# Kernel tuning notes

Hardware: AMD Instinct MI355X
Metric: run time of the kernel (lower is better)

Reference implementation:

```python
import jax, jax.numpy as jnp
import numpy as np

NEG_SLOPE = 0.2
EPS = 1e-16


def setup_inputs() -> dict:
    key = jax.random.key(0)
    k1, k2, k3, k4, k5 = jax.random.split(key, 5)
    N, E, F_IN, H, C = 100000, 1600000, 128, 4, 32
    x = jax.random.normal(k1, (N, F_IN), dtype=jnp.float32)
    edge_index = jax.random.randint(k2, (2, E), 0, N, dtype=jnp.int64)
    W = jax.random.normal(k3, (F_IN, H * C), dtype=jnp.float32) * (1.0 / np.sqrt(F_IN))
    att_src = jax.random.normal(k4, (H, C), dtype=jnp.float32) * 0.1
    att_dst = jax.random.normal(k5, (H, C), dtype=jnp.float32) * 0.1
    bias = jnp.zeros((H * C,), dtype=jnp.float32)
    return {"x": x, "edge_index": edge_index, "W": W, "att_src": att_src,
            "att_dst": att_dst, "bias": bias}


def reference(x, edge_index, W, att_src, att_dst, bias):
    N = x.shape[0]
    H, C = att_src.shape
    # PyG GATConv default: add self-loops
    loops = jnp.arange(N, dtype=edge_index.dtype)
    src = jnp.concatenate([edge_index[0], loops])  # [E+N]
    dst = jnp.concatenate([edge_index[1], loops])  # [E+N]

    h = (x @ W).reshape(N, H, C)                  # [N,H,C]
    a_src = jnp.einsum('nhc,hc->nh', h, att_src)  # [N,H]
    a_dst = jnp.einsum('nhc,hc->nh', h, att_dst)  # [N,H]

    e = a_src[src] + a_dst[dst]                   # [E',H]
    e = jax.nn.leaky_relu(e, NEG_SLOPE)

    # segment softmax over destination nodes (numerically stable)
    m = jax.ops.segment_max(e, dst, num_segments=N)      # [N,H]
    p = jnp.exp(e - m[dst])                               # [E',H]
    s = jax.ops.segment_sum(p, dst, num_segments=N)       # [N,H]
    alpha = p / (s[dst] + EPS)                             # [E',H]

    msg = h[src] * alpha[:, :, None]                       # [E',H,C]
    out = jax.ops.segment_sum(msg, dst, num_segments=N)   # [N,H,C]
    return out.reshape(N, H * C) + bias
```

## Files before the change

### kernel.cpp

```cpp
#include <hip/hip_runtime.h>
#include <stdint.h>


#define SLOT 64
#define CNTS 16
#define BCNS 16
#define BCAP 1536
#define MAXB 2048
#define KCH  8192
#define PST  68

typedef __attribute__((ext_vector_type(8))) _Float16 h8;
typedef __attribute__((ext_vector_type(4))) float    f4x;
typedef __attribute__((ext_vector_type(2))) unsigned u32x2;

__device__ __forceinline__ float b2f(unsigned short u) {
    union { unsigned int i; float f; } v; v.i = ((unsigned int)u) << 16; return v.f;
}
__device__ __forceinline__ unsigned short f2b(float f) {
    union { float f; unsigned int i; } v; v.f = f;
    unsigned int i = v.i;
    unsigned int r = (i + 0x7FFFu + ((i >> 16) & 1u)) >> 16;
    return (unsigned short)r;
}
__device__ __forceinline__ unsigned short f2h(float f) {
    union { _Float16 h; unsigned short u; } v; v.h = (_Float16)f; return v.u;
}
__device__ __forceinline__ float h2f(unsigned short u) {
    union { _Float16 h; unsigned short u; } v; v.u = u; return (float)v.h;
}

__device__ __forceinline__ int edge_at(const int* idx32, const long long* idx64,
                                       int is64, long long pos) {
    return is64 ? (int)idx64[pos] : idx32[pos];
}

__global__ void k_prep(const void* __restrict__ Wv, const void* __restrict__ asv,
                       const void* __restrict__ adv, const void* __restrict__ bv,
                       const int* __restrict__ eidx, const unsigned int* __restrict__ xw,
                       int* __restrict__ flags,
                       _Float16* __restrict__ Wth, _Float16* __restrict__ Wtl,
                       float* __restrict__ attf , float* __restrict__ biasf ,
                       int* __restrict__ bcnt, int nbcnt ) {
    __shared__ int nz, bf;
    int tid = threadIdx.x;
    if (tid == 0) { nz = 0; bf = 0; }
    __syncthreads();
    int hits = 0;
    for (int i = tid; i < 4096; i += 256) {
        unsigned int e = (xw[i] >> 7) & 0xFFu;
        if (e >= 0x60u && e < 0xA0u) ++hits;
    }
    atomicAdd(&bf, hits);
    if (blockIdx.x == 0) {
        int bad = 0;
        for (int i = tid; i < 1024; i += 256)
            if (eidx[2 * i + 1] != 0) bad = 1;
        if (bad) atomicOr(&nz, 1);
    }
    __syncthreads();
    int isbf = (bf > 3072) ? 1 : 0;
    if (blockIdx.x == 0 && tid == 0) {
        flags[0] = (nz == 0) ? 1 : 0;
        flags[1] = isbf;
    }
    for (int i = blockIdx.x * 256 + tid; i < nbcnt; i += gridDim.x * 256)
        bcnt[i] = 0;
    int gtid = blockIdx.x * 256 + tid;
    for (int i = gtid; i < 16384; i += gridDim.x * 256) {
        int col = i >> 7, k = i & 127;
        float w = isbf ? b2f(((const unsigned short*)Wv)[k * 128 + col])
                       : ((const float*)Wv)[k * 128 + col];
        unsigned short hi = f2h(w);
        unsigned short lo = f2h(w - h2f(hi));
        ((unsigned short*)Wth)[i] = hi;
        ((unsigned short*)Wtl)[i] = lo;
    }
    if (blockIdx.x == 0) {
        for (int i = tid; i < 128; i += 256) {
            attf[i]       = isbf ? b2f(((const unsigned short*)asv)[i]) : ((const float*)asv)[i];
            attf[128 + i] = isbf ? b2f(((const unsigned short*)adv)[i]) : ((const float*)adv)[i];
            biasf[i]      = isbf ? b2f(((const unsigned short*)bv)[i]) : ((const float*)bv)[i];
        }
    }
}

__global__ __launch_bounds__(256) void k_gemm_scatter(
    const void* __restrict__ xv,
    const _Float16* __restrict__ Wth, const _Float16* __restrict__ Wtl,
    const float* __restrict__ attf, const int* __restrict__ flags,
    unsigned short* __restrict__ hbf, float* __restrict__ asf,
    float* __restrict__ adf, int N,
    const int* __restrict__ idx32, const long long* __restrict__ idx64,
    int* __restrict__ bcnt, unsigned* __restrict__ bdat,
    int* __restrict__ cnt, int* __restrict__ esrc,
    int E, int Gg, int SB) {
    __shared__ unsigned short xsh[64 * 128];
    __shared__ unsigned short xsl[64 * 128];
    int tid = threadIdx.x;
    int bid = blockIdx.x;

    if (bid < SB) {
        int is64 = flags[0];
        int NBK = (N + 63) >> 6;
        long long e0 = (long long)bid * KCH;
        long long e1 = e0 + KCH; if (e1 > E) e1 = E;
        if (e0 >= E) return;

        if (NBK <= MAXB) {
            int wid = tid >> 6;
            int* h0 = (int*)xsh; int* h1 = h0 + MAXB;
            int* h2 = (int*)xsl; int* h3 = h2 + MAXB;
            int* hw = (wid == 0) ? h0 : (wid == 1) ? h1 : (wid == 2) ? h2 : h3;
            for (int i = tid; i < NBK; i += 256) { h0[i] = 0; h1[i] = 0; h2[i] = 0; h3[i] = 0; }
            __syncthreads();
            for (long long e = e0 + tid; e < e1; e += 256) {
                int d = is64 ? (int)idx64[(long long)E + e] : idx32[E + e];
                atomicAdd(&hw[d >> 6], 1);
            }
            __syncthreads();
            for (int b = tid; b < NBK; b += 256) {
                int c0 = h0[b], c1 = h1[b], c2 = h2[b], c3 = h3[b];
                int t = c0 + c1 + c2 + c3;
                int base = (t > 0) ? atomicAdd(&bcnt[(size_t)b * BCNS], t) : 0;
                h0[b] = base;
                h1[b] = base + c0;
                h2[b] = base + c0 + c1;
                h3[b] = base + c0 + c1 + c2;
            }
            __syncthreads();
            for (long long e = e0 + tid; e < e1; e += 256) {
                int d, s;
                if (is64) {
                    d = (int)idx64[(long long)E + e]; s = (int)idx64[e];
                } else {
                    d = idx32[E + e]; s = idx32[e];
                }
                int b = d >> 6;
                int p = atomicAdd(&hw[b], 1);
                if (p < BCAP)
                    bdat[(size_t)b * BCAP + p] = (unsigned)s | ((unsigned)(d & 63) << 26);
            }
        } else {
            for (long long e = e0 + tid; e < e1; e += 256) {
                int d = edge_at(idx32, idx64, is64, (long long)E + e);
                int s = edge_at(idx32, idx64, is64, e);
                int p = atomicAdd(&cnt[(size_t)d * CNTS], 1);
                if (p < SLOT) esrc[(size_t)d * SLOT + p] = s;
            }
        }
        return;
    }

    int rb = bid - SB;
    if (rb >= Gg) return;
    int r0 = rb * 64;
    int isbf = flags[1];
    int w = tid >> 6;
    int lane = tid & 63;
    int li = lane & 15;
    int g  = lane >> 4;
    int c0 = w * 32;

    h8 Bh[2][4], Bl[2][4];
#pragma unroll
    for (int t = 0; t < 2; ++t)
#pragma unroll
        for (int s = 0; s < 4; ++s) {
            size_t o = (size_t)(c0 + 16 * t + li) * 128 + 32 * s + 8 * g;
            Bh[t][s] = *(const h8*)(Wth + o);
            Bl[t][s] = *(const h8*)(Wtl + o);
        }

#pragma unroll
    for (int it = 0; it < 4; ++it) {
        int idx = it * 2048 + tid * 8;
        int r = idx >> 7, k = idx & 127;
        int gr = r0 + r; if (gr >= N) gr = N - 1;
        float v[8];
        if (isbf) {
            uint4 raw = *(const uint4*)((const unsigned short*)xv + (size_t)gr * 128 + k);
            v[0] = b2f((unsigned short)(raw.x & 0xFFFFu)); v[1] = b2f((unsigned short)(raw.x >> 16));
            v[2] = b2f((unsigned short)(raw.y & 0xFFFFu)); v[3] = b2f((unsigned short)(raw.y >> 16));
            v[4] = b2f((unsigned short)(raw.z & 0xFFFFu)); v[5] = b2f((unsigned short)(raw.z >> 16));
            v[6] = b2f((unsigned short)(raw.w & 0xFFFFu)); v[7] = b2f((unsigned short)(raw.w >> 16));
        } else {
            const float* xf = (const float*)xv;
            float4 a = *(const float4*)(xf + (size_t)gr * 128 + k);
            float4 b = *(const float4*)(xf + (size_t)gr * 128 + k + 4);
            v[0] = a.x; v[1] = a.y; v[2] = a.z; v[3] = a.w;
            v[4] = b.x; v[5] = b.y; v[6] = b.z; v[7] = b.w;
        }
        uint4 PH, PL;
        unsigned int ph[4], pl[4];
#pragma unroll
        for (int jj = 0; jj < 4; ++jj) {
            unsigned short h0 = f2h(v[2 * jj]), h1 = f2h(v[2 * jj + 1]);
            unsigned short l0 = f2h(v[2 * jj] - h2f(h0));
            unsigned short l1 = f2h(v[2 * jj + 1] - h2f(h1));
            ph[jj] = (unsigned int)h0 | ((unsigned int)h1 << 16);
            pl[jj] = (unsigned int)l0 | ((unsigned int)l1 << 16);
        }
        PH.x = ph[0]; PH.y = ph[1]; PH.z = ph[2]; PH.w = ph[3];
        PL.x = pl[0]; PL.y = pl[1]; PL.z = pl[2]; PL.w = pl[3];
        int off = r * 256 + ((2 * k) ^ ((r & 7) << 4));
        *(uint4*)((char*)xsh + off) = PH;
        *(uint4*)((char*)xsl + off) = PL;
    }
    __syncthreads();

    f4x acc[4][2];
#pragma unroll
    for (int m = 0; m < 4; ++m)
#pragma unroll
        for (int t = 0; t < 2; ++t) acc[m][t] = (f4x){0.f, 0.f, 0.f, 0.f};

#pragma unroll
    for (int s = 0; s < 4; ++s) {
#pragma unroll
        for (int m = 0; m < 4; ++m) {
            int row = 16 * m + li;
            int kb = (32 * s + 8 * g) * 2;
            int off = row * 256 + (kb ^ ((row & 7) << 4));
            h8 ah = *(const h8*)((const char*)xsh + off);
            h8 al = *(const h8*)((const char*)xsl + off);
#pragma unroll
            for (int t = 0; t < 2; ++t) {
                acc[m][t] = __builtin_amdgcn_mfma_f32_16x16x32_f16(ah, Bh[t][s], acc[m][t], 0, 0, 0);
                acc[m][t] = __builtin_amdgcn_mfma_f32_16x16x32_f16(al, Bh[t][s], acc[m][t], 0, 0, 0);
                acc[m][t] = __builtin_amdgcn_mfma_f32_16x16x32_f16(ah, Bl[t][s], acc[m][t], 0, 0, 0);
            }
        }
    }

    float at_s0 = attf[c0 + li],       at_s1 = attf[c0 + 16 + li];
    float at_d0 = attf[128 + c0 + li], at_d1 = attf[128 + c0 + 16 + li];
#pragma unroll
    for (int m = 0; m < 4; ++m) {
        float s1v[4], s2v[4];
#pragma unroll
        for (int j = 0; j < 4; ++j) {
            s1v[j] = acc[m][0][j] * at_s0 + acc[m][1][j] * at_s1;
            s2v[j] = acc[m][0][j] * at_d0 + acc[m][1][j] * at_d1;
        }
#pragma unroll
        for (int j = 0; j < 4; ++j) {
#pragma unroll
            for (int msk = 1; msk < 16; msk <<= 1) {
                s1v[j] += __shfl_xor(s1v[j], msk);
                s2v[j] += __shfl_xor(s2v[j], msk);
            }
        }
        if (li == 0) {
#pragma unroll
            for (int j = 0; j < 4; ++j) {
                int gr = r0 + 16 * m + 4 * g + j;
                if (gr < N) {
                    asf[(size_t)gr * 4 + w] = s1v[j];
                    adf[(size_t)gr * 4 + w] = s2v[j];
                }
            }
        }
    }

    __syncthreads();
#pragma unroll
    for (int m = 0; m < 4; ++m)
#pragma unroll
        for (int t = 0; t < 2; ++t)
#pragma unroll
            for (int j = 0; j < 4; ++j)
                xsh[(16 * m + 4 * g + j) * 128 + c0 + 16 * t + li] = f2b(acc[m][t][j]);
    __syncthreads();
#pragma unroll
    for (int it = 0; it < 4; ++it) {
        int u = it * 2048 + tid * 8;
        int r = u >> 7, k = u & 127;
        int gr = r0 + r;
        if (gr < N)
            *(uint4*)(hbf + (size_t)gr * 128 + k) = *(const uint4*)(xsh + u);
    }
}

template <int NB>
__device__ __forceinline__ void agg_node2(
    int n, int dl, int deg, int lane,
    const int lslot[64][SLOT], float* psh,
    const unsigned short* __restrict__ hbf,
    const float* __restrict__ asf, const float* __restrict__ adf,
    float a[4], float& invho) {
    int half = lane >> 5;
    int cl = lane & 31;
    int hd = cl >> 3;
    int sl = (lane == 0) ? n : ((lane <= deg) ? lslot[dl][lane - 1] : n);
    float4 av, adv;
    asm volatile("global_load_dwordx4 %0, %1, off"
                 : "=v"(av) : "v"((const void*)(asf + (size_t)sl * 4)));
    asm volatile("global_load_dwordx4 %0, %1, off"
                 : "=v"(adv) : "v"((const void*)(adf + (size_t)n * 4)));
    u32x2 vv[NB * 8];
#pragma unroll
    for (int k = 0; k < NB * 8; ++k) {
        int it = 2 * k + half;
        int s = (it == 0) ? n : ((it <= deg) ? lslot[dl][it - 1] : n);
        asm volatile("global_load_dwordx2 %0, %1, off"
                     : "=v"(vv[k]) : "v"((const void*)(hbf + (size_t)s * 128 + 4 * cl)));
    }
    asm volatile("s_waitcnt vmcnt(%0)" :: "n"(NB * 8));
    __builtin_amdgcn_sched_barrier(0);

    float p0 = 0.f, p1 = 0.f, p2 = 0.f, p3 = 0.f;
    if (lane <= deg) {
        float e0 = av.x + adv.x; e0 = fmaxf(e0, 0.2f * e0); p0 = __expf(e0);
        float e1 = av.y + adv.y; e1 = fmaxf(e1, 0.2f * e1); p1 = __expf(e1);
        float e2 = av.z + adv.z; e2 = fmaxf(e2, 0.2f * e2); p2 = __expf(e2);
        float e3 = av.w + adv.w; e3 = fmaxf(e3, 0.2f * e3); p3 = __expf(e3);
    }
    psh[0 * PST + lane] = p0; psh[1 * PST + lane] = p1;
    psh[2 * PST + lane] = p2; psh[3 * PST + lane] = p3;
    __builtin_amdgcn_wave_barrier();
    asm volatile("s_waitcnt lgkmcnt(0)" ::: "memory");
    __builtin_amdgcn_wave_barrier();

    float ps0 = p0, ps1 = p1, ps2 = p2, ps3 = p3;
#pragma unroll
    for (int m = 1; m < 64; m <<= 1) {
        ps0 += __shfl_xor(ps0, m);
        ps1 += __shfl_xor(ps1, m);
        ps2 += __shfl_xor(ps2, m);
        ps3 += __shfl_xor(ps3, m);
    }
    float den = hd == 0 ? ps0 : hd == 1 ? ps1 : hd == 2 ? ps2 : ps3;
    invho = 1.0f / (den + 1e-16f);

#pragma unroll
    for (int bi = 0; bi < NB; ++bi) {
        asm volatile("s_waitcnt vmcnt(%0)" :: "n"(8 * (NB - 1 - bi)));
        __builtin_amdgcn_sched_barrier(0);
#pragma unroll
        for (int k2 = 0; k2 < 8; ++k2) {
            int it = 2 * (bi * 8 + k2) + half;
            float q = psh[hd * PST + it];
            u32x2 v = vv[bi * 8 + k2];
            a[0] += q * b2f((unsigned short)v[0]);
            a[1] += q * b2f((unsigned short)(v[0] >> 16));
            a[2] += q * b2f((unsigned short)v[1]);
            a[3] += q * b2f((unsigned short)(v[1] >> 16));
        }
    }
}

__global__ __launch_bounds__(256) void k_bagg(
    const unsigned* __restrict__ bdat, const int* __restrict__ bcnt,
    const unsigned short* __restrict__ hbf,
    const float* __restrict__ asf, const float* __restrict__ adf,
    const int* __restrict__ idx32, const long long* __restrict__ idx64,
    const float* __restrict__ biasf, const int* __restrict__ flags,
    void* __restrict__ outv, int N, int E) {
    __shared__ int   lcnt[64];
    __shared__ int   lslot[64][SLOT];
    __shared__ float p_all[4][4 * PST];
    int b = blockIdx.x >> 1;
    int bh = blockIdx.x & 1;
    int tid = threadIdx.x;
    int wid = tid >> 6, lane = tid & 63, head = lane >> 4;

    if (tid < 64) lcnt[tid] = 0;
    __syncthreads();
    int mm = bcnt[(size_t)b * BCNS];
    int ovf = (mm > BCAP);
    if (mm > BCAP) mm = BCAP;
    for (int i = tid; i < mm; i += 256) {
        unsigned e = bdat[(size_t)b * BCAP + i];
        int dl = (int)(e >> 26);
        int p = atomicAdd(&lcnt[dl], 1);
        if (p < SLOT) lslot[dl][p] = (int)(e & 0x03FFFFFFu);
    }
    __syncthreads();

    int cl = lane & 31;
    float b0 = biasf[2 * lane], b1 = biasf[2 * lane + 1];
    float4 bq4 = *(const float4*)(biasf + 4 * cl);
    float* psh = p_all[wid];
    int isbf = flags[1];
    int is64 = flags[0];

    for (int u = 0; u < 8; ++u) {
        int dl = bh * 32 + wid * 8 + u;
        int n = (b << 6) + dl;
        if (n >= N) break;
        int deg = lcnt[dl];
        bool fb = ovf || (deg > SLOT - 1);

        if (!fb && deg <= 31) {
            float a4[4] = {0.f, 0.f, 0.f, 0.f};
            float invh = 0.f;
            int nb = (deg + 16) >> 4;
            if (nb == 1) agg_node2<1>(n, dl, deg, lane, lslot, psh, hbf, asf, adf, a4, invh);
            else         agg_node2<2>(n, dl, deg, lane, lslot, psh, hbf, asf, adf, a4, invh);
#pragma unroll
            for (int c = 0; c < 4; ++c) a4[c] += __shfl_xor(a4[c], 32);
            float o0 = a4[0] * invh + bq4.x, o1 = a4[1] * invh + bq4.y;
            float o2 = a4[2] * invh + bq4.z, o3 = a4[3] * invh + bq4.w;
            if (lane < 32) {
                if (isbf) {
                    u32x2 pk;
                    pk[0] = (unsigned)f2b(o0) | ((unsigned)f2b(o1) << 16);
                    pk[1] = (unsigned)f2b(o2) | ((unsigned)f2b(o3) << 16);
                    *(u32x2*)((unsigned*)outv + (size_t)n * 64 + cl * 2) = pk;
                } else {
                    float4 f4v; f4v.x = o0; f4v.y = o1; f4v.z = o2; f4v.w = o3;
                    *(float4*)((float*)outv + (size_t)n * 128 + cl * 4) = f4v;
                }
            }
        } else if (!fb) {
            float a0 = 0.f, a1 = 0.f;
            float4 adv = *(const float4*)(adf + (size_t)n * 4);
            int sl = (lane == 0) ? n : ((lane <= deg) ? lslot[dl][lane - 1] : n);
            float4 av = *(const float4*)(asf + (size_t)sl * 4);
            float p0 = 0.f, p1 = 0.f, p2 = 0.f, p3 = 0.f;
            if (lane <= deg) {
                float e0 = av.x + adv.x; e0 = fmaxf(e0, 0.2f * e0); p0 = __expf(e0);
                float e1 = av.y + adv.y; e1 = fmaxf(e1, 0.2f * e1); p1 = __expf(e1);
                float e2 = av.z + adv.z; e2 = fmaxf(e2, 0.2f * e2); p2 = __expf(e2);
                float e3 = av.w + adv.w; e3 = fmaxf(e3, 0.2f * e3); p3 = __expf(e3);
            }
            psh[0 * PST + lane] = p0; psh[1 * PST + lane] = p1;
            psh[2 * PST + lane] = p2; psh[3 * PST + lane] = p3;
            __builtin_amdgcn_wave_barrier();
            asm volatile("s_waitcnt lgkmcnt(0)" ::: "memory");
            __builtin_amdgcn_wave_barrier();
            float ps0 = p0, ps1 = p1, ps2 = p2, ps3 = p3;
#pragma unroll
            for (int m = 1; m < 64; m <<= 1) {
                ps0 += __shfl_xor(ps0, m);
                ps1 += __shfl_xor(ps1, m);
                ps2 += __shfl_xor(ps2, m);
                ps3 += __shfl_xor(ps3, m);
            }
            float den = head == 0 ? ps0 : head == 1 ? ps1 : head == 2 ? ps2 : ps3;
            float invh = 1.0f / (den + 1e-16f);
            int nb = (deg + 8) >> 3;
            for (int bi = 0; bi < nb; ++bi) {
                unsigned vt[8];
#pragma unroll
                for (int k2 = 0; k2 < 8; ++k2) {
                    int it = bi * 8 + k2;
                    int s = (it == 0) ? n : ((it <= deg) ? lslot[dl][it - 1] : n);
                    vt[k2] = *(const unsigned int*)(hbf + (size_t)s * 128 + 2 * lane);
                }
#pragma unroll
                for (int k2 = 0; k2 < 8; ++k2) {
                    float q = psh[head * PST + bi * 8 + k2];
                    a0 += q * b2f((unsigned short)vt[k2]);
                    a1 += q * b2f((unsigned short)(vt[k2] >> 16));
                }
            }
            a0 = a0 * invh + b0;
            a1 = a1 * invh + b1;
            if (isbf) {
                unsigned int pk = (unsigned int)f2b(a0) | ((unsigned int)f2b(a1) << 16);
                ((unsigned int*)outv)[(size_t)n * 64 + lane] = pk;
            } else {
                float2 f2; f2.x = a0; f2.y = a1;
                *(float2*)((float*)outv + (size_t)n * 128 + 2 * lane) = f2;
            }
        } else {
            float a0 = 0.f, a1 = 0.f;
            float4 adv = *(const float4*)(adf + (size_t)n * 4);
            float adh = head == 0 ? adv.x : head == 1 ? adv.y : head == 2 ? adv.z : adv.w;
            float den = 0.f;
            {
                float ev = asf[(size_t)n * 4 + head] + adh; ev = fmaxf(ev, 0.2f * ev);
                float p = __expf(ev);
                unsigned int v = *(const unsigned int*)(hbf + (size_t)n * 128 + 2 * lane);
                den += p;
                a0 += p * b2f((unsigned short)v);
                a1 += p * b2f((unsigned short)(v >> 16));
            }
            for (int e = 0; e < E; ++e) {
                int d = edge_at(idx32, idx64, is64, (long long)E + e);
                if (d == n) {
                    int s = edge_at(idx32, idx64, is64, e);
                    float ev = asf[(size_t)s * 4 + head] + adh; ev = fmaxf(ev, 0.2f * ev);
                    float p = __expf(ev);
                    unsigned int v = *(const unsigned int*)(hbf + (size_t)s * 128 + 2 * lane);
                    den += p;
                    a0 += p * b2f((unsigned short)v);
                    a1 += p * b2f((unsigned short)(v >> 16));
                }
            }
            float invh = 1.0f / (den + 1e-16f);
            a0 = a0 * invh + b0;
            a1 = a1 * invh + b1;
            if (isbf) {
                unsigned int pk = (unsigned int)f2b(a0) | ((unsigned int)f2b(a1) << 16);
                ((unsigned int*)outv)[(size_t)n * 64 + lane] = pk;
            } else {
                float2 f2; f2.x = a0; f2.y = a1;
                *(float2*)((float*)outv + (size_t)n * 128 + 2 * lane) = f2;
            }
        }
        __builtin_amdgcn_wave_barrier();
    }
}

__global__ __launch_bounds__(256) void k_aggregate(
    const unsigned short* __restrict__ hbf,
    const float* __restrict__ asf, const float* __restrict__ adf,
    const int* __restrict__ cnt, const int* __restrict__ esrc,
    const int* __restrict__ idx32, const long long* __restrict__ idx64,
    const float* __restrict__ biasf, const int* __restrict__ flags,
    void* __restrict__ outv, int N, int E) {
    __shared__ float p_sh_all[4][SLOT * 4];
    __shared__ int   s_sh_all[4][SLOT];
    int wid = threadIdx.x >> 6;
    int lane = threadIdx.x & 63;
    int n = blockIdx.x * 4 + wid;
    if (n >= N) n = N - 1;
    float* p_sh = p_sh_all[wid];
    int*   s_sh = s_sh_all[wid];
    int head = lane >> 4;

    int deg = cnt[(size_t)n * CNTS];
    float4 adv = *(const float4*)(adf + (size_t)n * 4);
    bool fb = (deg > SLOT - 1);

    float p0 = 0.f, p1 = 0.f, p2 = 0.f, p3 = 0.f;
    if (!fb && lane <= deg) {
        int s = (lane == 0) ? n : esrc[(size_t)n * SLOT + lane - 1];
        float4 av = *(const float4*)(asf + (size_t)s * 4);
        float e0 = av.x + adv.x; e0 = fmaxf(e0, 0.2f * e0); p0 = __expf(e0);
        float e1 = av.y + adv.y; e1 = fmaxf(e1, 0.2f * e1); p1 = __expf(e1);
        float e2 = av.z + adv.z; e2 = fmaxf(e2, 0.2f * e2); p2 = __expf(e2);
        float e3 = av.w + adv.w; e3 = fmaxf(e3, 0.2f * e3); p3 = __expf(e3);
        s_sh[lane] = s;
        p_sh[lane * 4 + 0] = p0; p_sh[lane * 4 + 1] = p1;
        p_sh[lane * 4 + 2] = p2; p_sh[lane * 4 + 3] = p3;
    }
    __syncthreads();

    float b0 = biasf[2 * lane], b1 = biasf[2 * lane + 1];
    float a0 = 0.f, a1 = 0.f, invh;

    if (!fb) {
        float ps0 = p0, ps1 = p1, ps2 = p2, ps3 = p3;
#pragma unroll
        for (int m = 1; m < 64; m <<= 1) {
            ps0 += __shfl_xor(ps0, m);
            ps1 += __shfl_xor(ps1, m);
            ps2 += __shfl_xor(ps2, m);
            ps3 += __shfl_xor(ps3, m);
        }
        float den = head == 0 ? ps0 : head == 1 ? ps1 : head == 2 ? ps2 : ps3;
        invh = 1.0f / (den + 1e-16f);

        int tot = deg + 1;
        int i = 0;
        for (; i + 3 < tot; i += 4) {
            int s0 = s_sh[i], s1 = s_sh[i + 1], s2 = s_sh[i + 2], s3 = s_sh[i + 3];
            float q0 = p_sh[i * 4 + head],       q1 = p_sh[(i + 1) * 4 + head];
            float q2 = p_sh[(i + 2) * 4 + head], q3 = p_sh[(i + 3) * 4 + head];
            unsigned int v0 = *(const unsigned int*)(hbf + (size_t)s0 * 128 + 2 * lane);
            unsigned int v1 = *(const unsigned int*)(hbf + (size_t)s1 * 128 + 2 * lane);
            unsigned int v2 = *(const unsigned int*)(hbf + (size_t)s2 * 128 + 2 * lane);
            unsigned int v3 = *(const unsigned int*)(hbf + (size_t)s3 * 128 + 2 * lane);
            a0 += q0 * b2f((unsigned short)v0) + q1 * b2f((unsigned short)v1)
                + q2 * b2f((unsigned short)v2) + q3 * b2f((unsigned short)v3);
            a1 += q0 * b2f((unsigned short)(v0 >> 16)) + q1 * b2f((unsigned short)(v1 >> 16))
                + q2 * b2f((unsigned short)(v2 >> 16)) + q3 * b2f((unsigned short)(v3 >> 16));
        }
        for (; i < tot; ++i) {
            int s0 = s_sh[i];
            float q0 = p_sh[i * 4 + head];
            unsigned int v0 = *(const unsigned int*)(hbf + (size_t)s0 * 128 + 2 * lane);
            a0 += q0 * b2f((unsigned short)v0);
            a1 += q0 * b2f((unsigned short)(v0 >> 16));
        }
    } else {
        int is64 = flags[0];
        float adh = head == 0 ? adv.x : head == 1 ? adv.y : head == 2 ? adv.z : adv.w;
        float den = 0.f;
        {
            float ev = asf[(size_t)n * 4 + head] + adh; ev = fmaxf(ev, 0.2f * ev);
            float p = __expf(ev);
            unsigned int v = *(const unsigned int*)(hbf + (size_t)n * 128 + 2 * lane);
            den += p;
            a0 += p * b2f((unsigned short)v);
            a1 += p * b2f((unsigned short)(v >> 16));
        }
        for (int e = 0; e < E; ++e) {
            int d = edge_at(idx32, idx64, is64, (long long)E + e);
            if (d == n) {
                int s = edge_at(idx32, idx64, is64, e);
                float ev = asf[(size_t)s * 4 + head] + adh; ev = fmaxf(ev, 0.2f * ev);
                float p = __expf(ev);
                unsigned int v = *(const unsigned int*)(hbf + (size_t)s * 128 + 2 * lane);
                den += p;
                a0 += p * b2f((unsigned short)v);
                a1 += p * b2f((unsigned short)(v >> 16));
            }
        }
        invh = 1.0f / (den + 1e-16f);
    }

    a0 = a0 * invh + b0;
    a1 = a1 * invh + b1;
    if (flags[1]) {
        unsigned int pk = (unsigned int)f2b(a0) | ((unsigned int)f2b(a1) << 16);
        ((unsigned int*)outv)[(size_t)n * 64 + lane] = pk;
    } else {
        float2 f2; f2.x = a0; f2.y = a1;
        *(float2*)((float*)outv + (size_t)n * 128 + 2 * lane) = f2;
    }
}

extern "C" void kernel_launch(void* const* d_in, const int* in_sizes, int n_in,
                              void* d_out, int out_size, void* d_ws, size_t ws_size,
                              hipStream_t stream) {
    const void*      xv    = d_in[0];
    const int*       idx32 = (const int*)d_in[1];
    const long long* idx64 = (const long long*)d_in[1];

    int N = in_sizes[0] / 128;
    int E = in_sizes[1] / 2;

    char* ws = (char*)d_ws;
    size_t o = 0;
    auto alloc = [&](size_t bytes) {
        size_t r = o; o += (bytes + 255) & ~(size_t)255; return r;
    };
    unsigned short* hbf = (unsigned short*)(ws + alloc((size_t)N * 128 * 2));
    _Float16* Wth = (_Float16*)(ws + alloc(16384 * 2));
    _Float16* Wtl = (_Float16*)(ws + alloc(16384 * 2));
    float* attf  = (float*)(ws + alloc(256 * 4));
    float* biasf = (float*)(ws + alloc(128 * 4));
    float* asf   = (float*)(ws + alloc((size_t)N * 4 * 4));
    float* adf   = (float*)(ws + alloc((size_t)N * 4 * 4));
    int* cnt     = (int*)(ws + alloc((size_t)N * CNTS * 4));
    int* flags   = (int*)(ws + alloc(256));
    int* esrc    = (int*)(ws + alloc((size_t)N * SLOT * 4));
    int NBK = (N + 63) >> 6;
    int* bcnt      = (int*)(ws + alloc((size_t)NBK * BCNS * 4));
    unsigned* bdat = (unsigned*)(ws + alloc((size_t)NBK * BCAP * 4));

    int Gg = (N + 63) / 64;
    int SB = (E + KCH - 1) / KCH;
    int NB = SB + Gg;

    k_prep<<<16, 256, 0, stream>>>(d_in[2], d_in[3], d_in[4], d_in[5],
                                   idx32, (const unsigned int*)xv, flags,
                                   Wth, Wtl, attf, biasf,
                                   bcnt, (NBK <= MAXB) ? NBK * BCNS : 0);
    if (NBK <= MAXB) {
        k_gemm_scatter<<<NB, 256, 0, stream>>>(xv, Wth, Wtl, attf, flags, hbf, asf, adf, N,
                                               idx32, idx64, bcnt, bdat, cnt, esrc, E, Gg, SB);
        k_bagg<<<NBK * 2, 256, 0, stream>>>(bdat, bcnt, hbf, asf, adf, idx32, idx64,
                                            biasf, flags, d_out, N, E);
    } else {
        hipMemsetAsync(cnt, 0, (size_t)N * CNTS * 4, stream);
        k_gemm_scatter<<<NB, 256, 0, stream>>>(xv, Wth, Wtl, attf, flags, hbf, asf, adf, N,
                                               idx32, idx64, bcnt, bdat, cnt, esrc, E, Gg, SB);
        k_aggregate<<<(N + 3) / 4, 256, 0, stream>>>(hbf, asf, adf, cnt, esrc, idx32, idx64,
                                                     biasf, flags, d_out, N, E);
    }
}
```

Baseline: 253.3 us.

## Process two destination nodes per wave with interleaved gather loads

```diff
diff --git a/kernel.cpp b/kernel.cpp
--- a/kernel.cpp
+++ b/kernel.cpp
@@ -350,7 +350,244 @@
     }
 }
 
-__global__ __launch_bounds__(256) void k_bagg(
+template <int NBA, int NBB>
+__device__ __forceinline__ void agg_node2_dual(
+    int nA, int dlA, int degA, int nB, int dlB, int degB, int lane,
+    const int lslot[64][SLOT], float* pshA, float* pshB,
+    const unsigned short* __restrict__ hbf,
+    const float* __restrict__ asf, const float* __restrict__ adf,
+    float aA[4], float aB[4], float& invhA, float& invhB) {
+    int half = lane >> 5;
+    int cl = lane & 31;
+    int hd = cl >> 3;
+    int slA = (lane == 0) ? nA : ((lane <= degA) ? lslot[dlA][lane - 1] : nA);
+    float4 avA, adA;
+    asm volatile("global_load_dwordx4 %0, %1, off"
+                 : "=v"(avA) : "v"((const void*)(asf + (size_t)slA * 4)));
+    asm volatile("global_load_dwordx4 %0, %1, off"
+                 : "=v"(adA) : "v"((const void*)(adf + (size_t)nA * 4)));
+    u32x2 vvA[NBA * 8];
+#pragma unroll
+    for (int k = 0; k < NBA * 8; ++k) {
+        int it = 2 * k + half;
+        int s = (it == 0) ? nA : ((it <= degA) ? lslot[dlA][it - 1] : nA);
+        asm volatile("global_load_dwordx2 %0, %1, off"
+                     : "=v"(vvA[k]) : "v"((const void*)(hbf + (size_t)s * 128 + 4 * cl)));
+    }
+    int slB = (lane == 0) ? nB : ((lane <= degB) ? lslot[dlB][lane - 1] : nB);
+    float4 avB, adB;
+    asm volatile("global_load_dwordx4 %0, %1, off"
+                 : "=v"(avB) : "v"((const void*)(asf + (size_t)slB * 4)));
+    asm volatile("global_load_dwordx4 %0, %1, off"
+                 : "=v"(adB) : "v"((const void*)(adf + (size_t)nB * 4)));
+    u32x2 vvB[NBB * 8];
+#pragma unroll
+    for (int k = 0; k < NBB * 8; ++k) {
+        int it = 2 * k + half;
+        int s = (it == 0) ? nB : ((it <= degB) ? lslot[dlB][it - 1] : nB);
+        asm volatile("global_load_dwordx2 %0, %1, off"
+                     : "=v"(vvB[k]) : "v"((const void*)(hbf + (size_t)s * 128 + 4 * cl)));
+    }
+    asm volatile("s_waitcnt vmcnt(%0)" :: "n"(NBA * 8 + NBB * 8 + 2));
+    __builtin_amdgcn_sched_barrier(0);
+    float pA0 = 0.f, pA1 = 0.f, pA2 = 0.f, pA3 = 0.f;
+    if (lane <= degA) {
+        float e0 = avA.x + adA.x; e0 = fmaxf(e0, 0.2f * e0); pA0 = __expf(e0);
+        float e1 = avA.y + adA.y; e1 = fmaxf(e1, 0.2f * e1); pA1 = __expf(e1);
+        float e2 = avA.z + adA.z; e2 = fmaxf(e2, 0.2f * e2); pA2 = __expf(e2);
+        float e3 = avA.w + adA.w; e3 = fmaxf(e3, 0.2f * e3); pA3 = __expf(e3);
+    }
+    pshA[0 * PST + lane] = pA0; pshA[1 * PST + lane] = pA1;
+    pshA[2 * PST + lane] = pA2; pshA[3 * PST + lane] = pA3;
+    asm volatile("s_waitcnt vmcnt(%0)" :: "n"(NBB * 8));
+    __builtin_amdgcn_sched_barrier(0);
+    float pB0 = 0.f, pB1 = 0.f, pB2 = 0.f, pB3 = 0.f;
+    if (lane <= degB) {
+        float e0 = avB.x + adB.x; e0 = fmaxf(e0, 0.2f * e0); pB0 = __expf(e0);
+        float e1 = avB.y + adB.y; e1 = fmaxf(e1, 0.2f * e1); pB1 = __expf(e1);
+        float e2 = avB.z + adB.z; e2 = fmaxf(e2, 0.2f * e2); pB2 = __expf(e2);
+        float e3 = avB.w + adB.w; e3 = fmaxf(e3, 0.2f * e3); pB3 = __expf(e3);
+    }
+    pshB[0 * PST + lane] = pB0; pshB[1 * PST + lane] = pB1;
+    pshB[2 * PST + lane] = pB2; pshB[3 * PST + lane] = pB3;
+    __builtin_amdgcn_wave_barrier();
+    asm volatile("s_waitcnt lgkmcnt(0)" ::: "memory");
+    __builtin_amdgcn_wave_barrier();
+
+    float sA0 = pA0, sA1 = pA1, sA2 = pA2, sA3 = pA3;
+    float sB0 = pB0, sB1 = pB1, sB2 = pB2, sB3 = pB3;
+#pragma unroll
+    for (int m = 1; m < 64; m <<= 1) {
+        sA0 += __shfl_xor(sA0, m); sB0 += __shfl_xor(sB0, m);
+        sA1 += __shfl_xor(sA1, m); sB1 += __shfl_xor(sB1, m);
+        sA2 += __shfl_xor(sA2, m); sB2 += __shfl_xor(sB2, m);
+        sA3 += __shfl_xor(sA3, m); sB3 += __shfl_xor(sB3, m);
+    }
+    float denA = hd == 0 ? sA0 : hd == 1 ? sA1 : hd == 2 ? sA2 : sA3;
+    float denB = hd == 0 ? sB0 : hd == 1 ? sB1 : hd == 2 ? sB2 : sB3;
+    invhA = 1.0f / (denA + 1e-16f);
+    invhB = 1.0f / (denB + 1e-16f);
+
+#pragma unroll
+    for (int bi = 0; bi < NBA; ++bi) {
+        asm volatile("s_waitcnt vmcnt(%0)" :: "n"(8 * (NBA - 1 - bi) + NBB * 8 + 2));
+        __builtin_amdgcn_sched_barrier(0);
+#pragma unroll
+        for (int k2 = 0; k2 < 8; ++k2) {
+            int it = 2 * (bi * 8 + k2) + half;
+            float q = pshA[hd * PST + it];
+            u32x2 v = vvA[bi * 8 + k2];
+            aA[0] += q * b2f((unsigned short)v[0]);
+            aA[1] += q * b2f((unsigned short)(v[0] >> 16));
+            aA[2] += q * b2f((unsigned short)v[1]);
+            aA[3] += q * b2f((unsigned short)(v[1] >> 16));
+        }
+    }
+#pragma unroll
+    for (int bi = 0; bi < NBB; ++bi) {
+        asm volatile("s_waitcnt vmcnt(%0)" :: "n"(8 * (NBB - 1 - bi)));
+        __builtin_amdgcn_sched_barrier(0);
+#pragma unroll
+        for (int k2 = 0; k2 < 8; ++k2) {
+            int it = 2 * (bi * 8 + k2) + half;
+            float q = pshB[hd * PST + it];
+            u32x2 v = vvB[bi * 8 + k2];
+            aB[0] += q * b2f((unsigned short)v[0]);
+            aB[1] += q * b2f((unsigned short)(v[0] >> 16));
+            aB[2] += q * b2f((unsigned short)v[1]);
+            aB[3] += q * b2f((unsigned short)(v[1] >> 16));
+        }
+    }
+}
+
+__device__ __forceinline__ void bagg_store_fast(
+    void* outv, int n, int lane, int cl, int isbf,
+    const float a4in[4], float invh, float4 bq4) {
+    float a0 = a4in[0], a1 = a4in[1], a2 = a4in[2], a3 = a4in[3];
+    a0 += __shfl_xor(a0, 32); a1 += __shfl_xor(a1, 32);
+    a2 += __shfl_xor(a2, 32); a3 += __shfl_xor(a3, 32);
+    float o0 = a0 * invh + bq4.x, o1 = a1 * invh + bq4.y;
+    float o2 = a2 * invh + bq4.z, o3 = a3 * invh + bq4.w;
+    if (lane < 32) {
+        if (isbf) {
+            u32x2 pk;
+            pk[0] = (unsigned)f2b(o0) | ((unsigned)f2b(o1) << 16);
+            pk[1] = (unsigned)f2b(o2) | ((unsigned)f2b(o3) << 16);
+            *(u32x2*)((unsigned*)outv + (size_t)n * 64 + cl * 2) = pk;
+        } else {
+            float4 f4v; f4v.x = o0; f4v.y = o1; f4v.z = o2; f4v.w = o3;
+            *(float4*)((float*)outv + (size_t)n * 128 + cl * 4) = f4v;
+        }
+    }
+}
+
+__device__ void bagg_one(
+    int n, int dl, int deg, bool fb,
+    int lane, int head, int cl,
+    const int lslot[64][SLOT], float* psh,
+    const unsigned short* __restrict__ hbf,
+    const float* __restrict__ asf, const float* __restrict__ adf,
+    const int* __restrict__ idx32, const long long* __restrict__ idx64,
+    float b0, float b1, float4 bq4, int isbf, int is64,
+    void* __restrict__ outv, int N, int E) {
+    if (!fb && deg <= 31) {
+        float a4[4] = {0.f, 0.f, 0.f, 0.f};
+        float invh = 0.f;
+        int nb = (deg + 16) >> 4;
+        if (nb == 1) agg_node2<1>(n, dl, deg, lane, lslot, psh, hbf, asf, adf, a4, invh);
+        else         agg_node2<2>(n, dl, deg, lane, lslot, psh, hbf, asf, adf, a4, invh);
+        bagg_store_fast(outv, n, lane, cl, isbf, a4, invh, bq4);
+    } else if (!fb) {
+        float a0 = 0.f, a1 = 0.f;
+        float4 adv = *(const float4*)(adf + (size_t)n * 4);
+        int sl = (lane == 0) ? n : ((lane <= deg) ? lslot[dl][lane - 1] : n);
+        float4 av = *(const float4*)(asf + (size_t)sl * 4);
+        float p0 = 0.f, p1 = 0.f, p2 = 0.f, p3 = 0.f;
+        if (lane <= deg) {
+            float e0 = av.x + adv.x; e0 = fmaxf(e0, 0.2f * e0); p0 = __expf(e0);
+            float e1 = av.y + adv.y; e1 = fmaxf(e1, 0.2f * e1); p1 = __expf(e1);
+            float e2 = av.z + adv.z; e2 = fmaxf(e2, 0.2f * e2); p2 = __expf(e2);
+            float e3 = av.w + adv.w; e3 = fmaxf(e3, 0.2f * e3); p3 = __expf(e3);
+        }
+        psh[0 * PST + lane] = p0; psh[1 * PST + lane] = p1;
+        psh[2 * PST + lane] = p2; psh[3 * PST + lane] = p3;
+        __builtin_amdgcn_wave_barrier();
+        asm volatile("s_waitcnt lgkmcnt(0)" ::: "memory");
+        __builtin_amdgcn_wave_barrier();
+        float ps0 = p0, ps1 = p1, ps2 = p2, ps3 = p3;
+#pragma unroll
+        for (int m = 1; m < 64; m <<= 1) {
+            ps0 += __shfl_xor(ps0, m);
+            ps1 += __shfl_xor(ps1, m);
+            ps2 += __shfl_xor(ps2, m);
+            ps3 += __shfl_xor(ps3, m);
+        }
+        float den = head == 0 ? ps0 : head == 1 ? ps1 : head == 2 ? ps2 : ps3;
+        float invh = 1.0f / (den + 1e-16f);
+        int nb = (deg + 8) >> 3;
+        for (int bi = 0; bi < nb; ++bi) {
+            unsigned vt[8];
+#pragma unroll
+            for (int k2 = 0; k2 < 8; ++k2) {
+                int it = bi * 8 + k2;
+                int s = (it == 0) ? n : ((it <= deg) ? lslot[dl][it - 1] : n);
+                vt[k2] = *(const unsigned int*)(hbf + (size_t)s * 128 + 2 * lane);
+            }
+#pragma unroll
+            for (int k2 = 0; k2 < 8; ++k2) {
+                float q = psh[head * PST + bi * 8 + k2];
+                a0 += q * b2f((unsigned short)vt[k2]);
+                a1 += q * b2f((unsigned short)(vt[k2] >> 16));
+            }
+        }
+        a0 = a0 * invh + b0;
+        a1 = a1 * invh + b1;
+        if (isbf) {
+            unsigned int pk = (unsigned int)f2b(a0) | ((unsigned int)f2b(a1) << 16);
+            ((unsigned int*)outv)[(size_t)n * 64 + lane] = pk;
+        } else {
+            float2 f2; f2.x = a0; f2.y = a1;
+            *(float2*)((float*)outv + (size_t)n * 128 + 2 * lane) = f2;
+        }
+    } else {
+        float a0 = 0.f, a1 = 0.f;
+        float4 adv = *(const float4*)(adf + (size_t)n * 4);
+        float adh = head == 0 ? adv.x : head == 1 ? adv.y : head == 2 ? adv.z : adv.w;
+        float den = 0.f;
+        {
+            float ev = asf[(size_t)n * 4 + head] + adh; ev = fmaxf(ev, 0.2f * ev);
+            float p = __expf(ev);
+            unsigned int v = *(const unsigned int*)(hbf + (size_t)n * 128 + 2 * lane);
+            den += p;
+            a0 += p * b2f((unsigned short)v);
+            a1 += p * b2f((unsigned short)(v >> 16));
+        }
+        for (int e = 0; e < E; ++e) {
+            int d = edge_at(idx32, idx64, is64, (long long)E + e);
+            if (d == n) {
+                int s = edge_at(idx32, idx64, is64, e);
+                float ev = asf[(size_t)s * 4 + head] + adh; ev = fmaxf(ev, 0.2f * ev);
+                float p = __expf(ev);
+                unsigned int v = *(const unsigned int*)(hbf + (size_t)s * 128 + 2 * lane);
+                den += p;
+                a0 += p * b2f((unsigned short)v);
+                a1 += p * b2f((unsigned short)(v >> 16));
+            }
+        }
+        float invh = 1.0f / (den + 1e-16f);
+        a0 = a0 * invh + b0;
+        a1 = a1 * invh + b1;
+        if (isbf) {
+            unsigned int pk = (unsigned int)f2b(a0) | ((unsigned int)f2b(a1) << 16);
+            ((unsigned int*)outv)[(size_t)n * 64 + lane] = pk;
+        } else {
+            float2 f2; f2.x = a0; f2.y = a1;
+            *(float2*)((float*)outv + (size_t)n * 128 + 2 * lane) = f2;
+        }
+    }
+}
+
+__global__ __launch_bounds__(256, 4) void k_bagg(
     const unsigned* __restrict__ bdat, const int* __restrict__ bcnt,
     const unsigned short* __restrict__ hbf,
     const float* __restrict__ asf, const float* __restrict__ adf,
@@ -359,7 +596,7 @@
     void* __restrict__ outv, int N, int E) {
     __shared__ int   lcnt[64];
     __shared__ int   lslot[64][SLOT];
-    __shared__ float p_all[4][4 * PST];
+    __shared__ float p_all[4][2][4 * PST];
     int b = blockIdx.x >> 1;
     int bh = blockIdx.x & 1;
     int tid = threadIdx.x;
@@ -381,125 +618,51 @@
     int cl = lane & 31;
     float b0 = biasf[2 * lane], b1 = biasf[2 * lane + 1];
     float4 bq4 = *(const float4*)(biasf + 4 * cl);
-    float* psh = p_all[wid];
+    float* pshA = &p_all[wid][0][0];
+    float* pshB = &p_all[wid][1][0];
     int isbf = flags[1];
     int is64 = flags[0];
 
-    for (int u = 0; u < 8; ++u) {
-        int dl = bh * 32 + wid * 8 + u;
-        int n = (b << 6) + dl;
-        if (n >= N) break;
-        int deg = lcnt[dl];
-        bool fb = ovf || (deg > SLOT - 1);
-
-        if (!fb && deg <= 31) {
-            float a4[4] = {0.f, 0.f, 0.f, 0.f};
-            float invh = 0.f;
-            int nb = (deg + 16) >> 4;
-            if (nb == 1) agg_node2<1>(n, dl, deg, lane, lslot, psh, hbf, asf, adf, a4, invh);
-            else         agg_node2<2>(n, dl, deg, lane, lslot, psh, hbf, asf, adf, a4, invh);
-#pragma unroll
-            for (int c = 0; c < 4; ++c) a4[c] += __shfl_xor(a4[c], 32);
-            float o0 = a4[0] * invh + bq4.x, o1 = a4[1] * invh + bq4.y;
-            float o2 = a4[2] * invh + bq4.z, o3 = a4[3] * invh + bq4.w;
-            if (lane < 32) {
-                if (isbf) {
-                    u32x2 pk;
-                    pk[0] = (unsigned)f2b(o0) | ((unsigned)f2b(o1) << 16);
-                    pk[1] = (unsigned)f2b(o2) | ((unsigned)f2b(o3) << 16);
-                    *(u32x2*)((unsigned*)outv + (size_t)n * 64 + cl * 2) = pk;
-                } else {
-                    float4 f4v; f4v.x = o0; f4v.y = o1; f4v.z = o2; f4v.w = o3;
-                    *(float4*)((float*)outv + (size_t)n * 128 + cl * 4) = f4v;
-                }
-            }
-        } else if (!fb) {
-            float a0 = 0.f, a1 = 0.f;
-            float4 adv = *(const float4*)(adf + (size_t)n * 4);
-            int sl = (lane == 0) ? n : ((lane <= deg) ? lslot[dl][lane - 1] : n);
-            float4 av = *(const float4*)(asf + (size_t)sl * 4);
-            float p0 = 0.f, p1 = 0.f, p2 = 0.f, p3 = 0.f;
-            if (lane <= deg) {
-                float e0 = av.x + adv.x; e0 = fmaxf(e0, 0.2f * e0); p0 = __expf(e0);
-                float e1 = av.y + adv.y; e1 = fmaxf(e1, 0.2f * e1); p1 = __expf(e1);
-                float e2 = av.z + adv.z; e2 = fmaxf(e2, 0.2f * e2); p2 = __expf(e2);
-                float e3 = av.w + adv.w; e3 = fmaxf(e3, 0.2f * e3); p3 = __expf(e3);
-            }
-            psh[0 * PST + lane] = p0; psh[1 * PST + lane] = p1;
-            psh[2 * PST + lane] = p2; psh[3 * PST + lane] = p3;
-            __builtin_amdgcn_wave_barrier();
-            asm volatile("s_waitcnt lgkmcnt(0)" ::: "memory");
-            __builtin_amdgcn_wave_barrier();
-            float ps0 = p0, ps1 = p1, ps2 = p2, ps3 = p3;
-#pragma unroll
-            for (int m = 1; m < 64; m <<= 1) {
-                ps0 += __shfl_xor(ps0, m);
-                ps1 += __shfl_xor(ps1, m);
-                ps2 += __shfl_xor(ps2, m);
-                ps3 += __shfl_xor(ps3, m);
-            }
-            float den = head == 0 ? ps0 : head == 1 ? ps1 : head == 2 ? ps2 : ps3;
-            float invh = 1.0f / (den + 1e-16f);
-            int nb = (deg + 8) >> 3;
-            for (int bi = 0; bi < nb; ++bi) {
-                unsigned vt[8];
-#pragma unroll
-                for (int k2 = 0; k2 < 8; ++k2) {
-                    int it = bi * 8 + k2;
-                    int s = (it == 0) ? n : ((it <= deg) ? lslot[dl][it - 1] : n);
-                    vt[k2] = *(const unsigned int*)(hbf + (size_t)s * 128 + 2 * lane);
-                }
-#pragma unroll
-                for (int k2 = 0; k2 < 8; ++k2) {
-                    float q = psh[head * PST + bi * 8 + k2];
-                    a0 += q * b2f((unsigned short)vt[k2]);
-                    a1 += q * b2f((unsigned short)(vt[k2] >> 16));
-                }
-            }
-            a0 = a0 * invh + b0;
-            a1 = a1 * invh + b1;
-            if (isbf) {
-                unsigned int pk = (unsigned int)f2b(a0) | ((unsigned int)f2b(a1) << 16);
-                ((unsigned int*)outv)[(size_t)n * 64 + lane] = pk;
-            } else {
-                float2 f2; f2.x = a0; f2.y = a1;
-                *(float2*)((float*)outv + (size_t)n * 128 + 2 * lane) = f2;
-            }
+    int dbase = bh * 32 + wid * 8;
+    for (int u = 0; u < 8; u += 2) {
+        int dlA = dbase + u;
+        int nA = (b << 6) + dlA;
+        if (nA >= N) break;
+        int dlB = dlA + 1;
+        int nB = nA + 1;
+        bool validB = (nB < N);
+        int degA = lcnt[dlA];
+        int degB = validB ? lcnt[dlB] : 0;
+        bool fbA = ovf || (degA > SLOT - 1);
+        bool fbB = ovf || (degB > SLOT - 1);
+        bool fastA = !fbA && (degA <= 31);
+        bool fastB = validB && !fbB && (degB <= 31);
+
+        if (fastA && fastB) {
+            float aA[4] = {0.f, 0.f, 0.f, 0.f}, aB[4] = {0.f, 0.f, 0.f, 0.f};
+            float invhA = 0.f, invhB = 0.f;
+            int nbA = (degA + 16) >> 4;
+            int nbB = (degB + 16) >> 4;
+            if (nbA == 1 && nbB == 1)
+                agg_node2_dual<1, 1>(nA, dlA, degA, nB, dlB, degB, lane, lslot,
+                                     pshA, pshB, hbf, asf, adf, aA, aB, invhA, invhB);
+            else if (nbA == 1)
+                agg_node2_dual<1, 2>(nA, dlA, degA, nB, dlB, degB, lane, lslot,
+                                     pshA, pshB, hbf, asf, adf, aA, aB, invhA, invhB);
+            else if (nbB == 1)
+                agg_node2_dual<2, 1>(nA, dlA, degA, nB, dlB, degB, lane, lslot,
+                                     pshA, pshB, hbf, asf, adf, aA, aB, invhA, invhB);
+            else
+                agg_node2_dual<2, 2>(nA, dlA, degA, nB, dlB, degB, lane, lslot,
+                                     pshA, pshB, hbf, asf, adf, aA, aB, invhA, invhB);
+            bagg_store_fast(outv, nA, lane, cl, isbf, aA, invhA, bq4);
+            bagg_store_fast(outv, nB, lane, cl, isbf, aB, invhB, bq4);
         } else {
-            float a0 = 0.f, a1 = 0.f;
-            float4 adv = *(const float4*)(adf + (size_t)n * 4);
-            float adh = head == 0 ? adv.x : head == 1 ? adv.y : head == 2 ? adv.z : adv.w;
-            float den = 0.f;
-            {
-                float ev = asf[(size_t)n * 4 + head] + adh; ev = fmaxf(ev, 0.2f * ev);
-                float p = __expf(ev);
-                unsigned int v = *(const unsigned int*)(hbf + (size_t)n * 128 + 2 * lane);
-                den += p;
-                a0 += p * b2f((unsigned short)v);
-                a1 += p * b2f((unsigned short)(v >> 16));
-            }
-            for (int e = 0; e < E; ++e) {
-                int d = edge_at(idx32, idx64, is64, (long long)E + e);
-                if (d == n) {
-                    int s = edge_at(idx32, idx64, is64, e);
-                    float ev = asf[(size_t)s * 4 + head] + adh; ev = fmaxf(ev, 0.2f * ev);
-                    float p = __expf(ev);
-                    unsigned int v = *(const unsigned int*)(hbf + (size_t)s * 128 + 2 * lane);
-                    den += p;
-                    a0 += p * b2f((unsigned short)v);
-                    a1 += p * b2f((unsigned short)(v >> 16));
-                }
-            }
-            float invh = 1.0f / (den + 1e-16f);
-            a0 = a0 * invh + b0;
-            a1 = a1 * invh + b1;
-            if (isbf) {
-                unsigned int pk = (unsigned int)f2b(a0) | ((unsigned int)f2b(a1) << 16);
-                ((unsigned int*)outv)[(size_t)n * 64 + lane] = pk;
-            } else {
-                float2 f2; f2.x = a0; f2.y = a1;
-                *(float2*)((float*)outv + (size_t)n * 128 + 2 * lane) = f2;
-            }
+            bagg_one(nA, dlA, degA, fbA, lane, head, cl, lslot, pshA,
+                     hbf, asf, adf, idx32, idx64, b0, b1, bq4, isbf, is64, outv, N, E);
+            if (validB)
+                bagg_one(nB, dlB, degB, fbB, lane, head, cl, lslot, pshA,
+                         hbf, asf, adf, idx32, idx64, b0, b1, bq4, isbf, is64, outv, N, E);
         }
         __builtin_amdgcn_wave_barrier();
     }
```

After: 275.8 us. 8.9% more time.
